# Kernel optimization log

Measured on AMD Instinct MI355X. Metric: run time of the kernel, lower is better.

The kernel has to match this reference:

```python
import jax, jax.numpy as jnp
import numpy as np

T, B, Y, X, C = 9, 2, 128, 128, 64
W = (T - 1) // 2
WIN, HEADS = 8, 4
EPS = 1e-3  # keras LayerNormalization default epsilon


def _get_indices(center, size):
    right = list(range(center, size, 2))
    left = list(range(center - 2, -1, -2))
    idx = np.array(left[::-1] + right, dtype=np.int32)
    return np.clip(idx, 1, size - 2)


def _pyramid_indices(t):
    levels = []
    size, center = t, (t - 1) // 2
    while size > 1:
        c = _get_indices(center, size)
        levels.append((c - 1, c, c + 1))
        center = int(np.where(c == center)[0][0])
        size = len(c)
    return levels


LEVELS = _pyramid_indices(T)            # 3 levels for T=9: sizes 5, 3, 1
CIN = [C * (l + 1) for l in range(len(LEVELS))]    # 64, 128, 192
COUT = [C * (l + 2) for l in range(len(LEVELS))]   # 128, 192, 256


def _window_attention(q, kv, wqkv, bqkv, wo, bo):
    # WindowSpatialAttention: non-overlapping WINxWIN windows, MHA of q over kv.
    N, Yd, Xd, Cd = q.shape
    w, h = WIN, HEADS
    dh = Cd // h
    nY, nX = Yd // w, Xd // w

    def to_win(t):
        t = t.reshape(N, nY, w, nX, w, Cd).transpose(0, 1, 3, 2, 4, 5)
        return t.reshape(N * nY * nX, w * w, Cd)

    qw, kvw = to_win(q), to_win(kv)
    qp = (qw @ wqkv[0] + bqkv[0]).reshape(-1, w * w, h, dh)
    kp = (kvw @ wqkv[1] + bqkv[1]).reshape(-1, w * w, h, dh)
    vp = (kvw @ wqkv[2] + bqkv[2]).reshape(-1, w * w, h, dh)
    logits = jnp.einsum('nqhd,nkhd->nhqk', qp, kp) / jnp.sqrt(jnp.float32(dh))
    attn = jax.nn.softmax(logits, axis=-1)
    out = jnp.einsum('nhqk,nkhd->nqhd', attn, vp).reshape(-1, w * w, Cd)
    out = out @ wo + bo
    out = out.reshape(N, nY, nX, w, w, Cd).transpose(0, 1, 3, 2, 4, 5)
    return out.reshape(N, Yd, Xd, Cd)


def _forward(x, params):
    fidx = np.arange(T) - W  # relative frame indices, static (non frame-aware)
    current = x
    level1 = None
    for l, (pi, ci, ni) in enumerate(LEVELS):
        emb, lng, lnb, wqkv, bqkv, wo, bo, cw, cb = params[l]
        cin = current.shape[-1]
        # additive relative temporal embedding, indexed by frame offset + W
        t_emb = emb[fidx + W]                       # [Tl, cin]
        cur = current + t_emb[:, None, None, None, :]
        mu = cur.mean(-1, keepdims=True)
        var = cur.var(-1, keepdims=True)
        cur = (cur - mu) * jax.lax.rsqrt(var + EPS) * lng + lnb
        S = len(ci)
        prev = cur[pi].reshape(S * B, Y, X, cin)
        cen = cur[ci].reshape(S * B, Y, X, cin)
        nxt = cur[ni].reshape(S * B, Y, X, cin)
        q = jnp.concatenate([cen, prev, cen, nxt], axis=0)
        kv = jnp.concatenate([prev, cen, nxt, cen], axis=0)
        att = _window_attention(q, kv, wqkv, bqkv, wo, bo)
        parts = jnp.split(att, 4, axis=0)           # SplitBatch(n_splits=4)
        comb = jnp.concatenate(parts, axis=-1)      # Combine: concat + 1x1 conv
        down = jax.nn.relu(comb @ cw + cb)
        if S > 1:
            down = down.reshape(S, B, Y, X, down.shape[-1])
        if l == 0:
            level1 = down
        current = down
        fidx = fidx[ci]
    return current, level1


def setup_inputs() -> dict:
    key = jax.random.key(0)
    ks = iter(jax.random.split(key, 64))
    inp = {'x': jax.random.normal(next(ks), (T, B, Y, X, C), jnp.float32)}
    for l, (ci, co) in enumerate(zip(CIN, COUT)):
        inp[f'emb{l}'] = 0.02 * jax.random.normal(next(ks), (T, ci), jnp.float32)
        inp[f'lng{l}'] = jnp.ones((ci,), jnp.float32)
        inp[f'lnb{l}'] = jnp.zeros((ci,), jnp.float32)
        inp[f'wqkv{l}'] = 0.02 * jax.random.normal(next(ks), (3, ci, ci), jnp.float32)
        inp[f'bqkv{l}'] = jnp.zeros((3, ci), jnp.float32)
        inp[f'wo{l}'] = 0.02 * jax.random.normal(next(ks), (ci, ci), jnp.float32)
        inp[f'bo{l}'] = jnp.zeros((ci,), jnp.float32)
        inp[f'cw{l}'] = 0.02 * jax.random.normal(next(ks), (4 * ci, co), jnp.float32)
        inp[f'cb{l}'] = jnp.zeros((co,), jnp.float32)
    return inp


def reference(x, emb0, lng0, lnb0, wqkv0, bqkv0, wo0, bo0, cw0, cb0,
              emb1, lng1, lnb1, wqkv1, bqkv1, wo1, bo1, cw1, cb1,
              emb2, lng2, lnb2, wqkv2, bqkv2, wo2, bo2, cw2, cb2):
    params = [
        (emb0, lng0, lnb0, wqkv0, bqkv0, wo0, bo0, cw0, cb0),
        (emb1, lng1, lnb1, wqkv1, bqkv1, wo1, bo1, cw1, cb1),
        (emb2, lng2, lnb2, wqkv2, bqkv2, wo2, bo2, cw2, cb2),
    ]
    return _forward(x, params)
```

## Files before the change

### kernel.cpp

```cpp
#include <hip/hip_runtime.h>

typedef _Float16 f16;
typedef f16 f16x4 __attribute__((ext_vector_type(4)));
typedef f16 f16x8 __attribute__((ext_vector_type(8)));
typedef float f32x4 __attribute__((ext_vector_type(4)));

#define MFMA16(a, b, c) __builtin_amdgcn_mfma_f32_16x16x16f16((a), (b), (c), 0, 0, 0)
#define MFMA32(a, b, c) __builtin_amdgcn_mfma_f32_16x16x32_f16((a), (b), (c), 0, 0, 0)

struct Meta   { int pi[5], ci[5], ni[5]; };
struct EmbMap { int m[9]; };

template <int CIN>
__global__ __launch_bounds__(256) void ln_kernel(
    const float* in, long lda, const float* __restrict__ emb,
    const float* __restrict__ lng, const float* __restrict__ lnb,
    f16* out, long ldo, EmbMap em) {
  long row = (long)blockIdx.x * 4 + (threadIdx.x >> 6);
  int t = (int)(row >> 15);
  int lane = threadIdx.x & 63;
  constexpr int NCH = CIN / 64;
  const float* xr = in + row * lda;
  const float* er = emb + (long)em.m[t] * CIN;
  float v[NCH];
  float s = 0.f;
#pragma unroll
  for (int i = 0; i < NCH; ++i) { int c = lane + (i << 6); v[i] = xr[c] + er[c]; s += v[i]; }
#pragma unroll
  for (int o = 32; o >= 1; o >>= 1) s += __shfl_xor(s, o);
  float mu = s * (1.f / CIN), ss = 0.f;
#pragma unroll
  for (int i = 0; i < NCH; ++i) { float d = v[i] - mu; ss += d * d; }
#pragma unroll
  for (int o = 32; o >= 1; o >>= 1) ss += __shfl_xor(ss, o);
  float inv = rsqrtf(ss * (1.f / CIN) + 1e-3f);
  f16* orow = out + row * ldo;
#pragma unroll
  for (int i = 0; i < NCH; ++i) {
    int c = lane + (i << 6);
    orow[c] = (f16)((v[i] - mu) * inv * lng[c] + lnb[c]);
  }
}

template <int CIN>
__global__ __launch_bounds__(64) void wT_kernel(const float* __restrict__ wqkv,
                                                f16* __restrict__ wqkvT) {
  int j = blockIdx.x;
  int which = j / CIN, jj = j % CIN;
  const float* src = wqkv + (long)which * CIN * CIN + jj;
  f16* dst = wqkvT + (long)j * CIN;
  for (int c = threadIdx.x; c < CIN; c += 64) dst[c] = (f16)src[(long)c * CIN];
}

template <int CIN, int CO>
__global__ __launch_bounds__(256) void woc_kernel(
    const float* __restrict__ wo, const float* __restrict__ bo,
    const float* __restrict__ cw, const float* __restrict__ cb,
    f16* __restrict__ wocA, float* __restrict__ fb) {
  __shared__ float scw[4 * CIN];
  __shared__ float red[256];
  int o = blockIdx.x;
  for (int i = threadIdx.x; i < 4 * CIN; i += 256) scw[i] = cw[(long)i * CO + o];
  __syncthreads();
  for (int pm = threadIdx.x; pm < 4 * CIN; pm += 256) {
    int p = pm / CIN, mm = pm % CIN;
    const float* wr = wo + (long)mm * CIN;
    const float* sc = scw + p * CIN;
    float s = 0.f;
    for (int c = 0; c < CIN; ++c) s += wr[c] * sc[c];
    wocA[((long)(pm >> 3) * CO + o) * 8 + (pm & 7)] = (f16)s;
  }
  float part = 0.f;
  for (int i = threadIdx.x; i < 4 * CIN; i += 256) part += bo[i % CIN] * scw[i];
  red[threadIdx.x] = part;
  __syncthreads();
  for (int st = 128; st > 0; st >>= 1) {
    if (threadIdx.x < st) red[threadIdx.x] += red[threadIdx.x + st];
    __syncthreads();
  }
  if (threadIdx.x == 0) fb[o] = cb[o] + red[0];
}

template <int CIN>
__global__ __launch_bounds__(256) void proj_kernel(
    const f16* __restrict__ cur, long lda, const f16* __restrict__ wT,
    const float* __restrict__ bqkv, f16* __restrict__ gq, f16* __restrict__ gk,
    f16* __restrict__ gvt) {
  constexpr int KS = CIN / 32;
  constexpr int NT = CIN / 16;
  constexpr int C8 = CIN / 8;
  __shared__ f16 sB[CIN * CIN];
  int which = blockIdx.x;
  long win = blockIdx.y;
  long img = win >> 8;
  int wid = (int)(win & 255);
  int wy = wid >> 4, wx = wid & 15;
  int w = threadIdx.x >> 6, lane = threadIdx.x & 63;
  int r16 = lane & 15, kq = lane >> 4;

  int tok = w * 16 + r16;
  long orig = img * 16384 + (long)(wy * 8 + (tok >> 3)) * 128 + wx * 8 + (tok & 7);
  const f16* arow = cur + orig * lda + kq * 8;
  f16x8 a[KS];
#pragma unroll
  for (int ks = 0; ks < KS; ++ks) a[ks] = *(const f16x8*)(arow + ks * 32);

  const f16* wsrc = wT + (long)which * CIN * CIN;
  for (int idx = threadIdx.x; idx < CIN * C8; idx += 256) {
    int j = idx / C8, c8 = idx % C8;
    f16x8 v = *(const f16x8*)(wsrc + idx * 8);
    int off = ((j * CIN + c8 * 8) * 2) ^ ((j & 7) << 4);
    *(f16x8*)((char*)sB + off) = v;
  }
  __syncthreads();

  f32x4 acc[NT] = {};
#pragma unroll
  for (int ks = 0; ks < KS; ++ks) {
#pragma unroll
    for (int t = 0; t < NT; ++t) {
      int off = (((t * 16 + r16) * CIN + ks * 32 + kq * 8) * 2) ^ ((r16 & 7) << 4);
      f16x8 bb = *(const f16x8*)((char*)sB + off);
      acc[t] = MFMA32(a[ks], bb, acc[t]);
    }
  }
  __syncthreads();

  if (which < 2) {
#pragma unroll
    for (int t = 0; t < NT; ++t) {
      float bias = bqkv[which * CIN + t * 16 + r16];
#pragma unroll
      for (int rg = 0; rg < 4; ++rg) {
        int r = w * 16 + kq * 4 + rg;
        int c = t * 16 + r16;
        int off = ((r * CIN + c) * 2) ^ ((r & 7) << 4);
        *(f16*)((char*)sB + off) = (f16)(acc[t][rg] + bias);
      }
    }
    __syncthreads();
    f16* dst = (which ? gk : gq) + win * 64 * CIN;
    for (int idx = threadIdx.x; idx < 64 * C8; idx += 256) {
      int r = idx / C8, c8 = idx % C8;
      int off = ((r * CIN + c8 * 8) * 2) ^ ((r & 7) << 4);
      f16x8 v = *(const f16x8*)((char*)sB + off);
      *(f16x8*)(dst + r * CIN + c8 * 8) = v;
    }
  } else {
#pragma unroll
    for (int t = 0; t < NT; ++t) {
      float bias = bqkv[2 * CIN + t * 16 + r16];
#pragma unroll
      for (int rg = 0; rg < 4; ++rg) {
        int c = t * 16 + r16;
        int pos = w * 16 + kq * 4 + rg;
        int off = ((c * 64 + pos) * 2) ^ ((c & 7) << 4);
        *(f16*)((char*)sB + off) = (f16)(acc[t][rg] + bias);
      }
    }
    __syncthreads();
    for (int c = threadIdx.x; c < CIN; c += 256) {
      f16* dst = gvt + (win * CIN + c) * 64;
#pragma unroll
      for (int p8 = 0; p8 < 8; ++p8) {
        int off = ((c * 64 + p8 * 8) * 2) ^ ((c & 7) << 4);
        *(f16x8*)(dst + p8 * 8) = *(const f16x8*)((char*)sB + off);
      }
    }
  }
}

template <int CIN, int DH, int CO>
__global__ __launch_bounds__(256) void attn4_kernel(
    const f16* __restrict__ gq, const f16* __restrict__ gk,
    const f16* __restrict__ gvt, const f16* __restrict__ wocA,
    const float* __restrict__ fb, float* __restrict__ out, Meta m) {
  constexpr int NKS = DH / 16;
  constexpr int NK8 = DH / 32;
  constexpr int NK4 = (DH % 32) / 16;
  constexpr int CO4 = CO / 4;
  constexpr int NTC = CO4 / 16;
  constexpr int NKD = 4 * CIN / 32;
  constexpr float scale = (DH == 16) ? 0.25f : (DH == 32) ? 0.1767766952966369f
                                                          : 0.1443375672974064f;
  constexpr float escale = scale * 1.4426950408889634f;
  __shared__ f16 O[4][64 * CIN];

  int img = blockIdx.y;
  int sidx = img >> 1, b = img & 1;
  int wid = blockIdx.x;
  int wy = wid >> 4, wx = wid & 15;
  int p = threadIdx.x >> 6, lane = threadIdx.x & 63;
  int r16 = lane & 15, kq = lane >> 4;
  int fpi = m.pi[sidx], fci = m.ci[sidx], fni = m.ni[sidx];

  int qfr = (p == 1) ? fpi : ((p == 3) ? fni : fci);
  int kfr = (p == 0) ? fpi : ((p == 2) ? fni : fci);
  long qwin = (long)((qfr * 2 + b) * 256 + wid);
  long kwin = (long)((kfr * 2 + b) * 256 + wid);
  char* Ob = (char*)O[p];

#pragma unroll
  for (int hh = 0; hh < 4; ++hh) {
    f16x8 kf8[4][NK8 ? NK8 : 1];
    f16x4 kf4[4][NK4 ? NK4 : 1];
#pragma unroll
    for (int tj = 0; tj < 4; ++tj) {
      const f16* kb = gk + (kwin * 64 + tj * 16 + r16) * CIN + hh * DH;
      if constexpr (NK8 > 0)
#pragma unroll
        for (int n = 0; n < NK8; ++n)
          kf8[tj][n] = *(const f16x8*)(kb + n * 32 + kq * 8);
      if constexpr (NK4 > 0)
#pragma unroll
        for (int n = 0; n < NK4; ++n)
          kf4[tj][n] = *(const f16x4*)(kb + NK8 * 32 + n * 16 + kq * 4);
    }
    f16x4 va[NKS][4];
#pragma unroll
    for (int dt = 0; dt < NKS; ++dt)
#pragma unroll
      for (int jt = 0; jt < 4; ++jt)
        va[dt][jt] = *(const f16x4*)(gvt + (kwin * CIN + hh * DH + dt * 16 + r16) * 64 +
                                     jt * 16 + kq * 4);

    f16x4 pa[4][4];
#pragma unroll
    for (int ti = 0; ti < 4; ++ti) {
      const f16* qb = gq + (qwin * 64 + ti * 16 + r16) * CIN + hh * DH;
      f32x4 s4[4] = {};
      if constexpr (NK8 > 0) {
        f16x8 qf8[NK8];
#pragma unroll
        for (int n = 0; n < NK8; ++n) qf8[n] = *(const f16x8*)(qb + n * 32 + kq * 8);
#pragma unroll
        for (int tj = 0; tj < 4; ++tj)
#pragma unroll
          for (int n = 0; n < NK8; ++n) s4[tj] = MFMA32(kf8[tj][n], qf8[n], s4[tj]);
      }
      if constexpr (NK4 > 0) {
        f16x4 qf4[NK4];
#pragma unroll
        for (int n = 0; n < NK4; ++n)
          qf4[n] = *(const f16x4*)(qb + NK8 * 32 + n * 16 + kq * 4);
#pragma unroll
        for (int tj = 0; tj < 4; ++tj)
#pragma unroll
          for (int n = 0; n < NK4; ++n) s4[tj] = MFMA16(kf4[tj][n], qf4[n], s4[tj]);
      }
      float sum = 0.f;
#pragma unroll
      for (int tj = 0; tj < 4; ++tj)
#pragma unroll
        for (int rg = 0; rg < 4; ++rg) {
          float e = __builtin_amdgcn_exp2f(s4[tj][rg] * escale);
          s4[tj][rg] = e;
          sum += e;
        }
      sum += __shfl_xor(sum, 16);
      sum += __shfl_xor(sum, 32);
      float inv = 1.f / sum;
#pragma unroll
      for (int tj = 0; tj < 4; ++tj) {
        f16x4 pv;
#pragma unroll
        for (int rg = 0; rg < 4; ++rg) pv[rg] = (f16)(s4[tj][rg] * inv);
        pa[tj][ti] = pv;
      }
    }

#pragma unroll
    for (int dt = 0; dt < NKS; ++dt) {
#pragma unroll
      for (int ti = 0; ti < 4; ++ti) {
        f32x4 po = {};
#pragma unroll
        for (int jt = 0; jt < 4; ++jt) po = MFMA16(va[dt][jt], pa[jt][ti], po);
        int i = ti * 16 + r16;
        int c0 = hh * DH + dt * 16 + kq * 4;
        f16x4 pk;
#pragma unroll
        for (int rg = 0; rg < 4; ++rg) pk[rg] = (f16)po[rg];
        int off = ((i * CIN + c0) * 2) ^ ((i & 7) << 4);
        *(f16x4*)(Ob + off) = pk;
      }
    }
  }
  __syncthreads();

  f32x4 dn[NTC][4] = {};
#pragma unroll
  for (int ck = 0; ck < NKD; ++ck) {
    int k0 = ck * 32;
    int psrc = k0 / CIN;
    int c = k0 - psrc * CIN;
    char* Osrc = (char*)O[psrc];
    f16x8 ob[4];
#pragma unroll
    for (int ti = 0; ti < 4; ++ti) {
      int i = ti * 16 + r16;
      int off = ((i * CIN + c + kq * 8) * 2) ^ ((i & 7) << 4);
      ob[ti] = *(const f16x8*)(Osrc + off);
    }
    long pm = (long)(k0 + kq * 8);
#pragma unroll
    for (int ot = 0; ot < NTC; ++ot) {
      f16x8 wa = *(const f16x8*)(wocA + ((pm >> 3) * CO + p * CO4 + ot * 16 + r16) * 8);
#pragma unroll
      for (int ti = 0; ti < 4; ++ti) dn[ot][ti] = MFMA32(wa, ob[ti], dn[ot][ti]);
    }
  }

#pragma unroll
  for (int ot = 0; ot < NTC; ++ot) {
    f32x4 fb4 = *(const f32x4*)(fb + p * CO4 + ot * 16 + kq * 4);
#pragma unroll
    for (int ti = 0; ti < 4; ++ti) {
      int i = ti * 16 + r16;
      long gtok = (long)img * 16384 + (wy * 8 + (i >> 3)) * 128 + wx * 8 + (i & 7);
      f32x4 v;
#pragma unroll
      for (int rg = 0; rg < 4; ++rg) v[rg] = fmaxf(dn[ot][ti][rg] + fb4[rg], 0.f);
      *(f32x4*)(out + gtok * CO + p * CO4 + ot * 16 + kq * 4) = v;
    }
  }
}

template <int CIN, int DH, int CO>
__global__ __launch_bounds__(256) void attn_kernel(
    const f16* __restrict__ gq, const f16* __restrict__ gk,
    const f16* __restrict__ gvt, const f16* __restrict__ wocA,
    const float* __restrict__ fb, float* __restrict__ out, Meta m) {
  constexpr int NKS = DH / 16;
  constexpr int NK8 = DH / 32;
  constexpr int NK4 = (DH % 32) / 16;
  constexpr int CO4 = CO / 4;
  constexpr int NTC = CO4 / 16;
  constexpr int NKD = CIN / 32;
  constexpr float scale = (DH == 16) ? 0.25f : (DH == 32) ? 0.1767766952966369f
                                                          : 0.1443375672974064f;
  constexpr float escale = scale * 1.4426950408889634f;
  __shared__ f16 O[2][64 * CIN];

  int img = blockIdx.y;
  int sidx = img >> 1, b = img & 1;
  int wid = blockIdx.x;
  int wy = wid >> 4, wx = wid & 15;
  int h = threadIdx.x >> 6, lane = threadIdx.x & 63;
  int r16 = lane & 15, kq = lane >> 4;
  int fpi = m.pi[sidx], fci = m.ci[sidx], fni = m.ni[sidx];

  f32x4 dn[NTC][4] = {};

#pragma unroll
  for (int p = 0; p < 4; ++p) {
    int qfr = (p == 1) ? fpi : ((p == 3) ? fni : fci);
    int kfr = (p == 0) ? fpi : ((p == 2) ? fni : fci);
    long qwin = (long)((qfr * 2 + b) * 256 + wid);
    long kwin = (long)((kfr * 2 + b) * 256 + wid);

    f16x8 kf8[4][NK8 ? NK8 : 1];
    f16x4 kf4[4][NK4 ? NK4 : 1];
#pragma unroll
    for (int tj = 0; tj < 4; ++tj) {
      const f16* kb = gk + (kwin * 64 + tj * 16 + r16) * CIN + h * DH;
      if constexpr (NK8 > 0)
#pragma unroll
        for (int n = 0; n < NK8; ++n)
          kf8[tj][n] = *(const f16x8*)(kb + n * 32 + kq * 8);
      if constexpr (NK4 > 0)
#pragma unroll
        for (int n = 0; n < NK4; ++n)
          kf4[tj][n] = *(const f16x4*)(kb + NK8 * 32 + n * 16 + kq * 4);
    }
    f16x4 va[NKS][4];
#pragma unroll
    for (int dt = 0; dt < NKS; ++dt)
#pragma unroll
      for (int jt = 0; jt < 4; ++jt)
        va[dt][jt] = *(const f16x4*)(gvt + (kwin * CIN + h * DH + dt * 16 + r16) * 64 +
                                     jt * 16 + kq * 4);

    f16x4 pa[4][4];
#pragma unroll
    for (int ti = 0; ti < 4; ++ti) {
      const f16* qb = gq + (qwin * 64 + ti * 16 + r16) * CIN + h * DH;
      f32x4 s4[4] = {};
      if constexpr (NK8 > 0) {
        f16x8 qf8[NK8];
#pragma unroll
        for (int n = 0; n < NK8; ++n) qf8[n] = *(const f16x8*)(qb + n * 32 + kq * 8);
#pragma unroll
        for (int tj = 0; tj < 4; ++tj)
#pragma unroll
          for (int n = 0; n < NK8; ++n) s4[tj] = MFMA32(kf8[tj][n], qf8[n], s4[tj]);
      }
      if constexpr (NK4 > 0) {
        f16x4 qf4[NK4];
#pragma unroll
        for (int n = 0; n < NK4; ++n)
          qf4[n] = *(const f16x4*)(qb + NK8 * 32 + n * 16 + kq * 4);
#pragma unroll
        for (int tj = 0; tj < 4; ++tj)
#pragma unroll
          for (int n = 0; n < NK4; ++n) s4[tj] = MFMA16(kf4[tj][n], qf4[n], s4[tj]);
      }
      float sum = 0.f;
#pragma unroll
      for (int tj = 0; tj < 4; ++tj)
#pragma unroll
        for (int rg = 0; rg < 4; ++rg) {
          float e = __builtin_amdgcn_exp2f(s4[tj][rg] * escale);
          s4[tj][rg] = e;
          sum += e;
        }
      sum += __shfl_xor(sum, 16);
      sum += __shfl_xor(sum, 32);
      float inv = 1.f / sum;
#pragma unroll
      for (int tj = 0; tj < 4; ++tj) {
        f16x4 pv;
#pragma unroll
        for (int rg = 0; rg < 4; ++rg) pv[rg] = (f16)(s4[tj][rg] * inv);
        pa[tj][ti] = pv;
      }
    }

    char* Ob = (char*)O[p & 1];
#pragma unroll
    for (int dt = 0; dt < NKS; ++dt) {
#pragma unroll
      for (int ti = 0; ti < 4; ++ti) {
        f32x4 po = {};
#pragma unroll
        for (int jt = 0; jt < 4; ++jt) po = MFMA16(va[dt][jt], pa[jt][ti], po);
        int i = ti * 16 + r16;
        int c0 = h * DH + dt * 16 + kq * 4;
        f16x4 pk;
#pragma unroll
        for (int rg = 0; rg < 4; ++rg) pk[rg] = (f16)po[rg];
        int off = ((i * CIN + c0) * 2) ^ ((i & 7) << 4);
        *(f16x4*)(Ob + off) = pk;
      }
    }
    __syncthreads();

#pragma unroll
    for (int ck = 0; ck < NKD; ++ck) {
      f16x8 ob[4];
#pragma unroll
      for (int ti = 0; ti < 4; ++ti) {
        int i = ti * 16 + r16;
        int off = ((i * CIN + ck * 32 + kq * 8) * 2) ^ ((i & 7) << 4);
        ob[ti] = *(const f16x8*)(Ob + off);
      }
      long pm = (long)(p * CIN + ck * 32 + kq * 8);
#pragma unroll
      for (int ot = 0; ot < NTC; ++ot) {
        f16x8 wa = *(const f16x8*)(wocA + ((pm >> 3) * CO + h * CO4 + ot * 16 + r16) * 8);
#pragma unroll
        for (int ti = 0; ti < 4; ++ti) dn[ot][ti] = MFMA32(wa, ob[ti], dn[ot][ti]);
      }
    }
  }

#pragma unroll
  for (int ot = 0; ot < NTC; ++ot) {
    f32x4 fb4 = *(const f32x4*)(fb + h * CO4 + ot * 16 + kq * 4);
#pragma unroll
    for (int ti = 0; ti < 4; ++ti) {
      int i = ti * 16 + r16;
      long gtok = (long)img * 16384 + (wy * 8 + (i >> 3)) * 128 + wx * 8 + (i & 7);
      f32x4 v;
#pragma unroll
      for (int rg = 0; rg < 4; ++rg) v[rg] = fmaxf(dn[ot][ti][rg] + fb4[rg], 0.f);
      *(f32x4*)(out + gtok * CO + h * CO4 + ot * 16 + kq * 4) = v;
    }
  }
}

extern "C" void kernel_launch(void* const* d_in, const int* in_sizes, int n_in,
                              void* d_out, int out_size, void* d_ws, size_t ws_size,
                              hipStream_t stream) {
  const float* x = (const float*)d_in[0];
#define PRM(l, k) ((const float*)d_in[1 + 9 * (l) + (k)])
  float* outCur = (float*)d_out;
  float* outL1 = (float*)d_out + 8388608;

  char* ws = (char*)d_ws;
  const size_t OFF_B = 125829120ull;
  const size_t OFF_W = OFF_B + 75497472ull;
  f16* qkvbase = (f16*)ws;
  char* wsB = ws + OFF_B;
  float* accum1 = (float*)wsB;
  f16* wqkvT = (f16*)(ws + OFF_W);
  f16* wocA = (f16*)(ws + OFF_W + 262144);
  float* fb = (float*)(ws + OFF_W + 262144 + 524288);

  Meta m0 = {{0, 1, 3, 5, 6}, {1, 2, 4, 6, 7}, {2, 3, 5, 7, 8}};
  Meta m1 = {{0, 1, 2, 0, 0}, {1, 2, 3, 0, 0}, {2, 3, 4, 0, 0}};
  Meta m2 = {{0, 0, 0, 0, 0}, {1, 0, 0, 0, 0}, {2, 0, 0, 0, 0}};
  EmbMap em0 = {{0, 1, 2, 3, 4, 5, 6, 7, 8}};
  EmbMap em1 = {{1, 2, 4, 6, 7, 0, 0, 0, 0}};
  EmbMap em2 = {{2, 4, 6, 0, 0, 0, 0, 0, 0}};

  {
    constexpr int CIN = 64, DH = 16, CO = 128, TL = 9, S = 5;
    long ntok = (long)TL * 2 * 16384;
    f16 *gq = qkvbase, *gk = gq + ntok * CIN, *gvt = gk + ntok * CIN;
    f16* cur = (f16*)wsB;
    ln_kernel<CIN><<<dim3((unsigned)(ntok / 4)), 256, 0, stream>>>(
        x, CIN, PRM(0, 0), PRM(0, 1), PRM(0, 2), cur, CIN, em0);
    wT_kernel<CIN><<<dim3(3 * CIN), 64, 0, stream>>>(PRM(0, 3), wqkvT);
    woc_kernel<CIN, CO><<<dim3(CO), 256, 0, stream>>>(PRM(0, 5), PRM(0, 6), PRM(0, 7), PRM(0, 8), wocA, fb);
    proj_kernel<CIN><<<dim3(3, (unsigned)(ntok / 64)), 256, 0, stream>>>(
        cur, CIN, wqkvT, PRM(0, 4), gq, gk, gvt);
    attn4_kernel<CIN, DH, CO><<<dim3(256, S * 2), 256, 0, stream>>>(
        gq, gk, gvt, wocA, fb, outL1, m0);
  }
  {
    constexpr int CIN = 128, DH = 32, CO = 192, TL = 5, S = 3;
    long ntok = (long)TL * 2 * 16384;
    f16 *gq = qkvbase, *gk = gq + ntok * CIN, *gvt = gk + ntok * CIN;
    f16* cur = (f16*)wsB;
    ln_kernel<CIN><<<dim3((unsigned)(ntok / 4)), 256, 0, stream>>>(
        outL1, CIN, PRM(1, 0), PRM(1, 1), PRM(1, 2), cur, CIN, em1);
    wT_kernel<CIN><<<dim3(3 * CIN), 64, 0, stream>>>(PRM(1, 3), wqkvT);
    woc_kernel<CIN, CO><<<dim3(CO), 256, 0, stream>>>(PRM(1, 5), PRM(1, 6), PRM(1, 7), PRM(1, 8), wocA, fb);
    proj_kernel<CIN><<<dim3(3, (unsigned)(ntok / 64)), 256, 0, stream>>>(
        cur, CIN, wqkvT, PRM(1, 4), gq, gk, gvt);
    attn4_kernel<CIN, DH, CO><<<dim3(256, S * 2), 256, 0, stream>>>(
        gq, gk, gvt, wocA, fb, accum1, m1);
  }
  {
    constexpr int CIN = 192, DH = 48, CO = 256, TL = 3, S = 1;
    long ntok = (long)TL * 2 * 16384;
    f16 *gq = qkvbase, *gk = gq + ntok * CIN, *gvt = gk + ntok * CIN;
    f16* cur = (f16*)accum1;
    ln_kernel<CIN><<<dim3((unsigned)(ntok / 4)), 256, 0, stream>>>(
        accum1, CIN, PRM(2, 0), PRM(2, 1), PRM(2, 2), cur, 384, em2);
    wT_kernel<CIN><<<dim3(3 * CIN), 64, 0, stream>>>(PRM(2, 3), wqkvT);
    woc_kernel<CIN, CO><<<dim3(CO), 256, 0, stream>>>(PRM(2, 5), PRM(2, 6), PRM(2, 7), PRM(2, 8), wocA, fb);
    proj_kernel<CIN><<<dim3(3, (unsigned)(ntok / 64)), 256, 0, stream>>>(
        cur, 384, wqkvT, PRM(2, 4), gq, gk, gvt);
    attn_kernel<CIN, DH, CO><<<dim3(256, S * 2), 256, 0, stream>>>(
        gq, gk, gvt, wocA, fb, outCur, m2);
  }
#undef PRM
}
```

Baseline: 656.4 us.

## Fuse LayerNorm into QKV projection and store level-1 intermediate in fp16

Merges the separate LayerNorm kernel into the projection kernel, so each block normalizes its 64 window tokens in registers and then loops over the Q, K and V weight matrices. This removes the fp16 normalized-activation buffer round trip, a kernel launch, and the threefold re-read of activations across the old 3-way grid split. The level-1 attention output is now written as fp16 instead of fp32, halving that intermediate's traffic. In exchange the fused kernel runs one-third as many blocks, each doing three sequential weight stages, and variance is computed as E[x²]−mu² with fp16-rounded inputs.

```diff
diff --git a/kernel.cpp b/kernel.cpp
--- a/kernel.cpp
+++ b/kernel.cpp
@@ -10,37 +10,6 @@
 
 struct Meta   { int pi[5], ci[5], ni[5]; };
 struct EmbMap { int m[9]; };
-
-template <int CIN>
-__global__ __launch_bounds__(256) void ln_kernel(
-    const float* in, long lda, const float* __restrict__ emb,
-    const float* __restrict__ lng, const float* __restrict__ lnb,
-    f16* out, long ldo, EmbMap em) {
-  long row = (long)blockIdx.x * 4 + (threadIdx.x >> 6);
-  int t = (int)(row >> 15);
-  int lane = threadIdx.x & 63;
-  constexpr int NCH = CIN / 64;
-  const float* xr = in + row * lda;
-  const float* er = emb + (long)em.m[t] * CIN;
-  float v[NCH];
-  float s = 0.f;
-#pragma unroll
-  for (int i = 0; i < NCH; ++i) { int c = lane + (i << 6); v[i] = xr[c] + er[c]; s += v[i]; }
-#pragma unroll
-  for (int o = 32; o >= 1; o >>= 1) s += __shfl_xor(s, o);
-  float mu = s * (1.f / CIN), ss = 0.f;
-#pragma unroll
-  for (int i = 0; i < NCH; ++i) { float d = v[i] - mu; ss += d * d; }
-#pragma unroll
-  for (int o = 32; o >= 1; o >>= 1) ss += __shfl_xor(ss, o);
-  float inv = rsqrtf(ss * (1.f / CIN) + 1e-3f);
-  f16* orow = out + row * ldo;
-#pragma unroll
-  for (int i = 0; i < NCH; ++i) {
-    int c = lane + (i << 6);
-    orow[c] = (f16)((v[i] - mu) * inv * lng[c] + lnb[c]);
-  }
-}
 
 template <int CIN>
 __global__ __launch_bounds__(64) void wT_kernel(const float* __restrict__ wqkv,
@@ -81,100 +50,142 @@
   if (threadIdx.x == 0) fb[o] = cb[o] + red[0];
 }
 
-template <int CIN>
-__global__ __launch_bounds__(256) void proj_kernel(
-    const f16* __restrict__ cur, long lda, const f16* __restrict__ wT,
-    const float* __restrict__ bqkv, f16* __restrict__ gq, f16* __restrict__ gk,
-    f16* __restrict__ gvt) {
+template <typename InT, int CIN>
+__global__ __launch_bounds__(256) void lnproj_kernel(
+    const InT* __restrict__ in, const float* __restrict__ emb,
+    const float* __restrict__ lng, const float* __restrict__ lnb,
+    const f16* __restrict__ wT, const float* __restrict__ bqkv,
+    f16* __restrict__ gq, f16* __restrict__ gk, f16* __restrict__ gvt,
+    EmbMap em) {
   constexpr int KS = CIN / 32;
   constexpr int NT = CIN / 16;
   constexpr int C8 = CIN / 8;
   __shared__ f16 sB[CIN * CIN];
-  int which = blockIdx.x;
-  long win = blockIdx.y;
+  long win = blockIdx.x;
   long img = win >> 8;
   int wid = (int)(win & 255);
   int wy = wid >> 4, wx = wid & 15;
   int w = threadIdx.x >> 6, lane = threadIdx.x & 63;
   int r16 = lane & 15, kq = lane >> 4;
-
   int tok = w * 16 + r16;
   long orig = img * 16384 + (long)(wy * 8 + (tok >> 3)) * 128 + wx * 8 + (tok & 7);
-  const f16* arow = cur + orig * lda + kq * 8;
+  const InT* arow = in + orig * CIN + kq * 8;
+  int t = (int)(img >> 1);
+  const float* er = emb + (long)em.m[t] * CIN + kq * 8;
+
+  float v[KS][8];
+  float s = 0.f, ssq = 0.f;
+#pragma unroll
+  for (int ks = 0; ks < KS; ++ks) {
+    f32x4 e0 = *(const f32x4*)(er + ks * 32);
+    f32x4 e1 = *(const f32x4*)(er + ks * 32 + 4);
+    if constexpr (sizeof(InT) == 4) {
+      f32x4 x0 = *(const f32x4*)((const float*)arow + ks * 32);
+      f32x4 x1 = *(const f32x4*)((const float*)arow + ks * 32 + 4);
+#pragma unroll
+      for (int j = 0; j < 4; ++j) { v[ks][j] = x0[j] + e0[j]; v[ks][4 + j] = x1[j] + e1[j]; }
+    } else {
+      f16x8 x = *(const f16x8*)((const f16*)arow + ks * 32);
+#pragma unroll
+      for (int j = 0; j < 4; ++j) { v[ks][j] = (float)x[j] + e0[j]; v[ks][4 + j] = (float)x[4 + j] + e1[j]; }
+    }
+#pragma unroll
+    for (int j = 0; j < 8; ++j) { s += v[ks][j]; ssq += v[ks][j] * v[ks][j]; }
+  }
+  s += __shfl_xor(s, 16);
+  s += __shfl_xor(s, 32);
+  ssq += __shfl_xor(ssq, 16);
+  ssq += __shfl_xor(ssq, 32);
+  float mu = s * (1.f / CIN);
+  float inv = rsqrtf(ssq * (1.f / CIN) - mu * mu + 1e-3f);
   f16x8 a[KS];
 #pragma unroll
-  for (int ks = 0; ks < KS; ++ks) a[ks] = *(const f16x8*)(arow + ks * 32);
-
-  const f16* wsrc = wT + (long)which * CIN * CIN;
-  for (int idx = threadIdx.x; idx < CIN * C8; idx += 256) {
-    int j = idx / C8, c8 = idx % C8;
-    f16x8 v = *(const f16x8*)(wsrc + idx * 8);
-    int off = ((j * CIN + c8 * 8) * 2) ^ ((j & 7) << 4);
-    *(f16x8*)((char*)sB + off) = v;
-  }
-  __syncthreads();
-
-  f32x4 acc[NT] = {};
-#pragma unroll
   for (int ks = 0; ks < KS; ++ks) {
-#pragma unroll
-    for (int t = 0; t < NT; ++t) {
-      int off = (((t * 16 + r16) * CIN + ks * 32 + kq * 8) * 2) ^ ((r16 & 7) << 4);
-      f16x8 bb = *(const f16x8*)((char*)sB + off);
-      acc[t] = MFMA32(a[ks], bb, acc[t]);
-    }
-  }
-  __syncthreads();
-
-  if (which < 2) {
-#pragma unroll
-    for (int t = 0; t < NT; ++t) {
-      float bias = bqkv[which * CIN + t * 16 + r16];
-#pragma unroll
-      for (int rg = 0; rg < 4; ++rg) {
-        int r = w * 16 + kq * 4 + rg;
-        int c = t * 16 + r16;
-        int off = ((r * CIN + c) * 2) ^ ((r & 7) << 4);
-        *(f16*)((char*)sB + off) = (f16)(acc[t][rg] + bias);
-      }
+    f32x4 g0 = *(const f32x4*)(lng + ks * 32 + kq * 8);
+    f32x4 g1 = *(const f32x4*)(lng + ks * 32 + kq * 8 + 4);
+    f32x4 b0 = *(const f32x4*)(lnb + ks * 32 + kq * 8);
+    f32x4 b1 = *(const f32x4*)(lnb + ks * 32 + kq * 8 + 4);
+#pragma unroll
+    for (int j = 0; j < 4; ++j) {
+      a[ks][j] = (f16)((v[ks][j] - mu) * inv * g0[j] + b0[j]);
+      a[ks][4 + j] = (f16)((v[ks][4 + j] - mu) * inv * g1[j] + b1[j]);
+    }
+  }
+
+#pragma unroll
+  for (int which = 0; which < 3; ++which) {
+    if (which) __syncthreads();
+    const f16* wsrc = wT + (long)which * CIN * CIN;
+    for (int idx = threadIdx.x; idx < CIN * C8; idx += 256) {
+      int j = idx / C8, c8 = idx % C8;
+      f16x8 vv = *(const f16x8*)(wsrc + idx * 8);
+      int off = ((j * CIN + c8 * 8) * 2) ^ ((j & 7) << 4);
+      *(f16x8*)((char*)sB + off) = vv;
     }
     __syncthreads();
-    f16* dst = (which ? gk : gq) + win * 64 * CIN;
-    for (int idx = threadIdx.x; idx < 64 * C8; idx += 256) {
-      int r = idx / C8, c8 = idx % C8;
-      int off = ((r * CIN + c8 * 8) * 2) ^ ((r & 7) << 4);
-      f16x8 v = *(const f16x8*)((char*)sB + off);
-      *(f16x8*)(dst + r * CIN + c8 * 8) = v;
-    }
-  } else {
-#pragma unroll
-    for (int t = 0; t < NT; ++t) {
-      float bias = bqkv[2 * CIN + t * 16 + r16];
-#pragma unroll
-      for (int rg = 0; rg < 4; ++rg) {
-        int c = t * 16 + r16;
-        int pos = w * 16 + kq * 4 + rg;
-        int off = ((c * 64 + pos) * 2) ^ ((c & 7) << 4);
-        *(f16*)((char*)sB + off) = (f16)(acc[t][rg] + bias);
+
+    f32x4 acc[NT] = {};
+#pragma unroll
+    for (int ks = 0; ks < KS; ++ks) {
+#pragma unroll
+      for (int tt = 0; tt < NT; ++tt) {
+        int off = (((tt * 16 + r16) * CIN + ks * 32 + kq * 8) * 2) ^ ((r16 & 7) << 4);
+        f16x8 bb = *(const f16x8*)((char*)sB + off);
+        acc[tt] = MFMA32(a[ks], bb, acc[tt]);
       }
     }
     __syncthreads();
-    for (int c = threadIdx.x; c < CIN; c += 256) {
-      f16* dst = gvt + (win * CIN + c) * 64;
-#pragma unroll
-      for (int p8 = 0; p8 < 8; ++p8) {
-        int off = ((c * 64 + p8 * 8) * 2) ^ ((c & 7) << 4);
-        *(f16x8*)(dst + p8 * 8) = *(const f16x8*)((char*)sB + off);
+
+    if (which < 2) {
+#pragma unroll
+      for (int tt = 0; tt < NT; ++tt) {
+        float bias = bqkv[which * CIN + tt * 16 + r16];
+#pragma unroll
+        for (int rg = 0; rg < 4; ++rg) {
+          int r = w * 16 + kq * 4 + rg;
+          int c = tt * 16 + r16;
+          int off = ((r * CIN + c) * 2) ^ ((r & 7) << 4);
+          *(f16*)((char*)sB + off) = (f16)(acc[tt][rg] + bias);
+        }
+      }
+      __syncthreads();
+      f16* dst = (which ? gk : gq) + win * 64 * CIN;
+      for (int idx = threadIdx.x; idx < 64 * C8; idx += 256) {
+        int r = idx / C8, c8 = idx % C8;
+        int off = ((r * CIN + c8 * 8) * 2) ^ ((r & 7) << 4);
+        f16x8 vv = *(const f16x8*)((char*)sB + off);
+        *(f16x8*)(dst + r * CIN + c8 * 8) = vv;
+      }
+    } else {
+#pragma unroll
+      for (int tt = 0; tt < NT; ++tt) {
+        float bias = bqkv[2 * CIN + tt * 16 + r16];
+#pragma unroll
+        for (int rg = 0; rg < 4; ++rg) {
+          int c = tt * 16 + r16;
+          int pos = w * 16 + kq * 4 + rg;
+          int off = ((c * 64 + pos) * 2) ^ ((c & 7) << 4);
+          *(f16*)((char*)sB + off) = (f16)(acc[tt][rg] + bias);
+        }
+      }
+      __syncthreads();
+      for (int c = threadIdx.x; c < CIN; c += 256) {
+        f16* dst = gvt + (win * CIN + c) * 64;
+#pragma unroll
+        for (int p8 = 0; p8 < 8; ++p8) {
+          int off = ((c * 64 + p8 * 8) * 2) ^ ((c & 7) << 4);
+          *(f16x8*)(dst + p8 * 8) = *(const f16x8*)((char*)sB + off);
+        }
       }
     }
   }
 }
 
-template <int CIN, int DH, int CO>
+template <int CIN, int DH, int CO, typename OutT>
 __global__ __launch_bounds__(256) void attn4_kernel(
     const f16* __restrict__ gq, const f16* __restrict__ gk,
     const f16* __restrict__ gvt, const f16* __restrict__ wocA,
-    const float* __restrict__ fb, float* __restrict__ out, Meta m) {
+    const float* __restrict__ fb, OutT* __restrict__ out, Meta m) {
   constexpr int NKS = DH / 16;
   constexpr int NK8 = DH / 32;
   constexpr int NK4 = (DH % 32) / 16;
@@ -259,12 +270,12 @@
         }
       sum += __shfl_xor(sum, 16);
       sum += __shfl_xor(sum, 32);
-      float inv = 1.f / sum;
+      float invs = 1.f / sum;
 #pragma unroll
       for (int tj = 0; tj < 4; ++tj) {
         f16x4 pv;
 #pragma unroll
-        for (int rg = 0; rg < 4; ++rg) pv[rg] = (f16)(s4[tj][rg] * inv);
+        for (int rg = 0; rg < 4; ++rg) pv[rg] = (f16)(s4[tj][rg] * invs);
         pa[tj][ti] = pv;
       }
     }
@@ -318,10 +329,17 @@
     for (int ti = 0; ti < 4; ++ti) {
       int i = ti * 16 + r16;
       long gtok = (long)img * 16384 + (wy * 8 + (i >> 3)) * 128 + wx * 8 + (i & 7);
-      f32x4 v;
-#pragma unroll
-      for (int rg = 0; rg < 4; ++rg) v[rg] = fmaxf(dn[ot][ti][rg] + fb4[rg], 0.f);
-      *(f32x4*)(out + gtok * CO + p * CO4 + ot * 16 + kq * 4) = v;
+      if constexpr (sizeof(OutT) == 4) {
+        f32x4 vv;
+#pragma unroll
+        for (int rg = 0; rg < 4; ++rg) vv[rg] = fmaxf(dn[ot][ti][rg] + fb4[rg], 0.f);
+        *(f32x4*)((float*)out + gtok * CO + p * CO4 + ot * 16 + kq * 4) = vv;
+      } else {
+        f16x4 vv;
+#pragma unroll
+        for (int rg = 0; rg < 4; ++rg) vv[rg] = (f16)fmaxf(dn[ot][ti][rg] + fb4[rg], 0.f);
+        *(f16x4*)((f16*)out + gtok * CO + p * CO4 + ot * 16 + kq * 4) = vv;
+      }
     }
   }
 }
@@ -416,12 +434,12 @@
         }
       sum += __shfl_xor(sum, 16);
       sum += __shfl_xor(sum, 32);
-      float inv = 1.f / sum;
+      float invs = 1.f / sum;
 #pragma unroll
       for (int tj = 0; tj < 4; ++tj) {
         f16x4 pv;
 #pragma unroll
-        for (int rg = 0; rg < 4; ++rg) pv[rg] = (f16)(s4[tj][rg] * inv);
+        for (int rg = 0; rg < 4; ++rg) pv[rg] = (f16)(s4[tj][rg] * invs);
         pa[tj][ti] = pv;
       }
     }
@@ -471,10 +489,10 @@
     for (int ti = 0; ti < 4; ++ti) {
       int i = ti * 16 + r16;
       long gtok = (long)img * 16384 + (wy * 8 + (i >> 3)) * 128 + wx * 8 + (i & 7);
-      f32x4 v;
-#pragma unroll
-      for (int rg = 0; rg < 4; ++rg) v[rg] = fmaxf(dn[ot][ti][rg] + fb4[rg], 0.f);
-      *(f32x4*)(out + gtok * CO + h * CO4 + ot * 16 + kq * 4) = v;
+      f32x4 vv;
+#pragma unroll
+      for (int rg = 0; rg < 4; ++rg) vv[rg] = fmaxf(dn[ot][ti][rg] + fb4[rg], 0.f);
+      *(f32x4*)(out + gtok * CO + h * CO4 + ot * 16 + kq * 4) = vv;
     }
   }
 }
@@ -491,8 +509,7 @@
   const size_t OFF_B = 125829120ull;
   const size_t OFF_W = OFF_B + 75497472ull;
   f16* qkvbase = (f16*)ws;
-  char* wsB = ws + OFF_B;
-  float* accum1 = (float*)wsB;
+  f16* accum1 = (f16*)(ws + OFF_B);
   f16* wqkvT = (f16*)(ws + OFF_W);
   f16* wocA = (f16*)(ws + OFF_W + 262144);
   float* fb = (float*)(ws + OFF_W + 262144 + 524288);
@@ -508,41 +525,32 @@
     constexpr int CIN = 64, DH = 16, CO = 128, TL = 9, S = 5;
     long ntok = (long)TL * 2 * 16384;
     f16 *gq = qkvbase, *gk = gq + ntok * CIN, *gvt = gk + ntok * CIN;
-    f16* cur = (f16*)wsB;
-    ln_kernel<CIN><<<dim3((unsigned)(ntok / 4)), 256, 0, stream>>>(
-        x, CIN, PRM(0, 0), PRM(0, 1), PRM(0, 2), cur, CIN, em0);
     wT_kernel<CIN><<<dim3(3 * CIN), 64, 0, stream>>>(PRM(0, 3), wqkvT);
     woc_kernel<CIN, CO><<<dim3(CO), 256, 0, stream>>>(PRM(0, 5), PRM(0, 6), PRM(0, 7), PRM(0, 8), wocA, fb);
-    proj_kernel<CIN><<<dim3(3, (unsigned)(ntok / 64)), 256, 0, stream>>>(
-        cur, CIN, wqkvT, PRM(0, 4), gq, gk, gvt);
-    attn4_kernel<CIN, DH, CO><<<dim3(256, S * 2), 256, 0, stream>>>(
+    lnproj_kernel<float, CIN><<<dim3((unsigned)(ntok / 64)), 256, 0, stream>>>(
+        x, PRM(0, 0), PRM(0, 1), PRM(0, 2), wqkvT, PRM(0, 4), gq, gk, gvt, em0);
+    attn4_kernel<CIN, DH, CO, float><<<dim3(256, S * 2), 256, 0, stream>>>(
         gq, gk, gvt, wocA, fb, outL1, m0);
   }
   {
     constexpr int CIN = 128, DH = 32, CO = 192, TL = 5, S = 3;
     long ntok = (long)TL * 2 * 16384;
     f16 *gq = qkvbase, *gk = gq + ntok * CIN, *gvt = gk + ntok * CIN;
-    f16* cur = (f16*)wsB;
-    ln_kernel<CIN><<<dim3((unsigned)(ntok / 4)), 256, 0, stream>>>(
-        outL1, CIN, PRM(1, 0), PRM(1, 1), PRM(1, 2), cur, CIN, em1);
     wT_kernel<CIN><<<dim3(3 * CIN), 64, 0, stream>>>(PRM(1, 3), wqkvT);
     woc_kernel<CIN, CO><<<dim3(CO), 256, 0, stream>>>(PRM(1, 5), PRM(1, 6), PRM(1, 7), PRM(1, 8), wocA, fb);
-    proj_kernel<CIN><<<dim3(3, (unsigned)(ntok / 64)), 256, 0, stream>>>(
-        cur, CIN, wqkvT, PRM(1, 4), gq, gk, gvt);
-    attn4_kernel<CIN, DH, CO><<<dim3(256, S * 2), 256, 0, stream>>>(
+    lnproj_kernel<float, CIN><<<dim3((unsigned)(ntok / 64)), 256, 0, stream>>>(
+        outL1, PRM(1, 0), PRM(1, 1), PRM(1, 2), wqkvT, PRM(1, 4), gq, gk, gvt, em1);
+    attn4_kernel<CIN, DH, CO, f16><<<dim3(256, S * 2), 256, 0, stream>>>(
         gq, gk, gvt, wocA, fb, accum1, m1);
   }
   {
     constexpr int CIN = 192, DH = 48, CO = 256, TL = 3, S = 1;
     long ntok = (long)TL * 2 * 16384;
     f16 *gq = qkvbase, *gk = gq + ntok * CIN, *gvt = gk + ntok * CIN;
-    f16* cur = (f16*)accum1;
-    ln_kernel<CIN><<<dim3((unsigned)(ntok / 4)), 256, 0, stream>>>(
-        accum1, CIN, PRM(2, 0), PRM(2, 1), PRM(2, 2), cur, 384, em2);
     wT_kernel<CIN><<<dim3(3 * CIN), 64, 0, stream>>>(PRM(2, 3), wqkvT);
     woc_kernel<CIN, CO><<<dim3(CO), 256, 0, stream>>>(PRM(2, 5), PRM(2, 6), PRM(2, 7), PRM(2, 8), wocA, fb);
-    proj_kernel<CIN><<<dim3(3, (unsigned)(ntok / 64)), 256, 0, stream>>>(
-        cur, 384, wqkvT, PRM(2, 4), gq, gk, gvt);
+    lnproj_kernel<f16, CIN><<<dim3((unsigned)(ntok / 64)), 256, 0, stream>>>(
+        accum1, PRM(2, 0), PRM(2, 1), PRM(2, 2), wqkvT, PRM(2, 4), gq, gk, gvt, em2);
     attn_kernel<CIN, DH, CO><<<dim3(256, S * 2), 256, 0, stream>>>(
         gq, gk, gvt, wocA, fb, outCur, m2);
   }
```

Result: slower. 684.7 us (+4.3%).
